# Optimization experiments

Hardware: AMD Instinct MI355X
Metric: run time of the kernel (lower is better)

The kernel has to match this reference:

```python
import jax, jax.numpy as jnp
import numpy as np

N = 100000      # nodes
E = 1600000     # edges
F_IN = 256      # num_features
H = 128         # hidden_dim
C = 16          # num_classes
LOG_SIGMA0 = float(np.log(0.1))  # prior_sigma = 0.1


def setup_inputs() -> dict:
    key = jax.random.key(0)
    ks = jax.random.split(key, 8)
    x = jax.random.normal(ks[0], (N, F_IN), jnp.float32)
    edge_index = jax.random.randint(ks[1], (2, E), 0, N, dtype=jnp.int64)
    # GCNConv linear weight + bias
    W = jax.random.normal(ks[2], (F_IN, H), jnp.float32) / np.float32(np.sqrt(F_IN))
    gcn_b = jnp.zeros((H,), jnp.float32)
    # BayesLinear params (mu + log_sigma) and fixed sampled noise eps
    w_mu = jax.random.normal(ks[3], (C, H), jnp.float32) / np.float32(np.sqrt(H))
    w_log_sigma = jnp.full((C, H), LOG_SIGMA0, jnp.float32)
    b_mu = jnp.zeros((C,), jnp.float32)
    b_log_sigma = jnp.full((C,), LOG_SIGMA0, jnp.float32)
    eps_w = jax.random.normal(ks[4], (C, H), jnp.float32)
    eps_b = jax.random.normal(ks[5], (C,), jnp.float32)
    return {"x": x, "edge_index": edge_index, "W": W, "gcn_b": gcn_b,
            "w_mu": w_mu, "w_log_sigma": w_log_sigma,
            "b_mu": b_mu, "b_log_sigma": b_log_sigma,
            "eps_w": eps_w, "eps_b": eps_b}


def reference(x, edge_index, W, gcn_b, w_mu, w_log_sigma, b_mu, b_log_sigma, eps_w, eps_b):
    n = x.shape[0]
    # --- GCNConv: add self-loops, symmetric deg^{-1/2} normalization ---
    loop = jnp.arange(n, dtype=edge_index.dtype)
    src = jnp.concatenate([edge_index[0], loop])  # message source j
    dst = jnp.concatenate([edge_index[1], loop])  # aggregation target i
    deg = jax.ops.segment_sum(jnp.ones_like(dst, dtype=x.dtype), dst, num_segments=n)
    deg_inv_sqrt = jnp.where(deg > 0, jax.lax.rsqrt(deg), 0.0)
    norm = deg_inv_sqrt[src] * deg_inv_sqrt[dst]            # [E+N]
    h = x @ W                                               # [N,H] transform first
    msg = h[src] * norm[:, None]                            # [E+N,H] gather
    agg = jax.ops.segment_sum(msg, dst, num_segments=n)     # [N,H] scatter-add
    agg = agg + gcn_b
    # --- ReLU; dropout is identity in eval mode ---
    a = jax.nn.relu(agg)
    # --- BayesLinear: w = mu + exp(log_sigma) * eps ---
    w = w_mu + jnp.exp(w_log_sigma) * eps_w                 # [C,H]
    b = b_mu + jnp.exp(b_log_sigma) * eps_b                 # [C]
    logits = a @ w.T + b                                    # [N,C]
    return jax.nn.log_softmax(logits, axis=1)
```

## Files before the change

### kernel.cpp

```cpp
#include <hip/hip_runtime.h>
#include <hip/hip_bf16.h>

#define N_NODES 100000
#define F_IN    256
#define H_DIM   128
#define C_CLS   16
#define NB_SCAN ((N_NODES + 255) / 256)
#define NSHARD  8
#define SHARD_W ((N_NODES + NSHARD - 1) / NSHARD)

typedef __attribute__((ext_vector_type(8))) short  short8;
typedef __attribute__((ext_vector_type(4))) float  float4v;
typedef __attribute__((ext_vector_type(4))) unsigned short ushort4v;

__device__ __forceinline__ float b2f(ushort u) {
    union { unsigned int i; float f; } v;
    v.i = ((unsigned int)u) << 16;
    return v.f;
}

__device__ __forceinline__ ushort f2b(float f) {
    unsigned int x = __float_as_uint(f);
    unsigned int r = (x + 0x7FFFu + ((x >> 16) & 1u)) >> 16;
    return (ushort)r;
}

__device__ __forceinline__ float ldsel(const void* p, int i, int f32f) {
    return f32f ? ((const float*)p)[i] : b2f(((const ushort*)p)[i]);
}

__global__ __launch_bounds__(64) void sniff(const ushort* __restrict__ x,
                                            const int* __restrict__ ei,
                                            int* __restrict__ flags) {
    int lane = threadIdx.x;
    int cnt_bf = 0;
#pragma unroll
    for (int j = 0; j < 4; ++j) {
        ushort u = x[lane * 4 + j];
        int e = (u >> 7) & 0xFF;
        if ((e >= 100 && e <= 140) || (u & 0x7FFF) == 0) cnt_bf++;
    }
    int zodd = (ei[2 * lane + 1] == 0) ? 1 : 0;
#pragma unroll
    for (int off = 32; off >= 1; off >>= 1) {
        cnt_bf += __shfl_xor(cnt_bf, off, 64);
        zodd   += __shfl_xor(zodd,   off, 64);
    }
    if (lane == 0) {
        flags[0] = (cnt_bf < 230) ? 1 : 0;
        flags[1] = (zodd  >= 32) ? 1 : 0;
    }
}

__global__ __launch_bounds__(256) void prep_params(const int* __restrict__ flags,
                                                   const void* __restrict__ W_any,
                                                   ushort* __restrict__ wtg,
                                                   const void* __restrict__ w_mu,
                                                   const void* __restrict__ w_ls,
                                                   const void* __restrict__ eps_w,
                                                   const void* __restrict__ b_mu,
                                                   const void* __restrict__ b_ls,
                                                   const void* __restrict__ eps_b,
                                                   const void* __restrict__ gcn_b,
                                                   ushort* __restrict__ whi,
                                                   ushort* __restrict__ wlo,
                                                   float* __restrict__ bias16,
                                                   float* __restrict__ gcnb_f) {
    const int f32f = flags[0];
    const int t = threadIdx.x;
    if (blockIdx.x < H_DIM) {
        const int n = blockIdx.x;
        float v = f32f ? ((const float*)W_any)[t * H_DIM + n]
                       : b2f(((const ushort*)W_any)[t * H_DIM + n]);
        wtg[n * F_IN + t] = f2b(v);
        return;
    }
#pragma unroll
    for (int i = t; i < C_CLS * H_DIM; i += 256) {
        float v = ldsel(w_mu, i, f32f) + __expf(ldsel(w_ls, i, f32f)) * ldsel(eps_w, i, f32f);
        ushort h = f2b(v);
        whi[i] = h;
        wlo[i] = f2b(v - b2f(h));
    }
    if (t < C_CLS)
        bias16[t] = ldsel(b_mu, t, f32f) + __expf(ldsel(b_ls, t, f32f)) * ldsel(eps_b, t, f32f);
    if (t < H_DIM)
        gcnb_f[t] = ldsel(gcn_b, t, f32f);
}

__global__ __launch_bounds__(256) void prep(const int* __restrict__ flags,
                                            const int* __restrict__ ei,
                                            int* __restrict__ cnt, int E) {
    int e = blockIdx.x * 256 + threadIdx.x;
    if (e >= E) return;
    int d = flags[1] ? ei[2L * E + 2L * e] : ei[(long)E + e];
    atomicAdd(&cnt[d], 1);
}

__global__ __launch_bounds__(256) void scan1(const int* __restrict__ cnt,
                                             int* __restrict__ offs,
                                             int* __restrict__ bsum) {
    __shared__ int sd[256];
    int t = threadIdx.x;
    int i = blockIdx.x * 256 + t;
    int v = (i < N_NODES) ? cnt[i] : 0;
    sd[t] = v;
    __syncthreads();
#pragma unroll
    for (int d = 1; d < 256; d <<= 1) {
        int add = (t >= d) ? sd[t - d] : 0;
        __syncthreads();
        sd[t] += add;
        __syncthreads();
    }
    if (i < N_NODES) offs[i] = sd[t] - v;
    if (t == 255) bsum[blockIdx.x] = sd[255];
}

__global__ __launch_bounds__(512) void scan2(const int* __restrict__ bsum,
                                             int* __restrict__ boff) {
    __shared__ int sd[512];
    int t = threadIdx.x;
    int v = (t < NB_SCAN) ? bsum[t] : 0;
    sd[t] = v;
    __syncthreads();
#pragma unroll
    for (int d = 1; d < 512; d <<= 1) {
        int add = (t >= d) ? sd[t - d] : 0;
        __syncthreads();
        sd[t] += add;
        __syncthreads();
    }
    if (t < NB_SCAN) boff[t] = sd[t] - v;
}

__global__ __launch_bounds__(256) void scan3(int* __restrict__ offs,
                                             const int* __restrict__ boff,
                                             const int* __restrict__ cnt,
                                             int* __restrict__ cursor,
                                             float* __restrict__ dis, int E) {
    int i = blockIdx.x * 256 + threadIdx.x;
    if (i == 0) offs[N_NODES] = E;
    if (i >= N_NODES) return;
    int off = offs[i] + boff[i >> 8];
    offs[i] = off;
    cursor[i] = off;
    dis[i] = rsqrtf((float)(cnt[i] + 1));
}

__global__ __launch_bounds__(256) void build_perm(const int* __restrict__ flags,
                                                  const int* __restrict__ ei,
                                                  int* __restrict__ cursor,
                                                  int* __restrict__ perm, int E) {
    const int shard = blockIdx.x & (NSHARD - 1);
    const int jb    = blockIdx.x >> 3;
    const int nb    = gridDim.x >> 3;
    const int lo = shard * SHARD_W;
    const int hi = lo + SHARD_W;
    const int i64 = flags[1];
    for (long e = (long)jb * 256 + threadIdx.x; e < E; e += (long)nb * 256) {
        int d = i64 ? ei[2L * E + 2L * e] : ei[(long)E + e];
        if (d >= lo && d < hi) {
            int s = i64 ? ei[2L * e] : ei[e];
            int slot = atomicAdd(&cursor[d], 1);
            perm[slot] = s;
        }
    }
}

__global__ __launch_bounds__(256) void gemm_xw(const int* __restrict__ flags,
                                               const void* __restrict__ x_any,
                                               const ushort* __restrict__ wtg,
                                               const float* __restrict__ dis,
                                               ushort* __restrict__ hout) {
    __shared__ __align__(16) ushort wt[128 * 128];
    const int f32f = flags[0];

    const int tid  = threadIdx.x;
    const int lane = tid & 63;
    const int quad = lane >> 4;
    const int lm   = lane & 15;
    const int wave = tid >> 6;

    const int rbase = blockIdx.x * 128 + wave * 32;
    int arow0 = rbase + lm;
    int arow1 = rbase + 16 + lm;
    if (arow0 >= N_NODES) arow0 = N_NODES - 1;
    if (arow1 >= N_NODES) arow1 = N_NODES - 1;
    const float*  xrf0 = (const float*) x_any + (size_t)arow0 * F_IN;
    const float*  xrf1 = (const float*) x_any + (size_t)arow1 * F_IN;
    const ushort* xrb0 = (const ushort*)x_any + (size_t)arow0 * F_IN;
    const ushort* xrb1 = (const ushort*)x_any + (size_t)arow1 * F_IN;

    float4v acc0[8], acc1[8];
#pragma unroll
    for (int c = 0; c < 8; ++c) {
        acc0[c] = (float4v){0.f, 0.f, 0.f, 0.f};
        acc1[c] = (float4v){0.f, 0.f, 0.f, 0.f};
    }

    for (int hh = 0; hh < 2; ++hh) {
        if (hh) __syncthreads();
#pragma unroll
        for (int it = 0; it < 8; ++it) {
            int flat = (it * 256 + tid) * 8;
            int col  = flat >> 7;
            int kloc = flat & 127;
            short8 v = *(const short8*)(wtg + col * F_IN + hh * 128 + kloc);
            int dst = ((col << 7) | kloc) ^ ((col & 7) << 3);
            *(short8*)(wt + dst) = v;
        }
        __syncthreads();
#pragma unroll
        for (int s = 0; s < 4; ++s) {
            int klocal = s * 32 + quad * 8;
            short8 afrag0, afrag1;
            if (f32f) {
                const float* p0 = xrf0 + hh * 128 + klocal;
                const float* p1 = xrf1 + hh * 128 + klocal;
                float4 u0 = *(const float4*)p0;
                float4 u1 = *(const float4*)(p0 + 4);
                float4 u2 = *(const float4*)p1;
                float4 u3 = *(const float4*)(p1 + 4);
                afrag0[0] = (short)f2b(u0.x); afrag0[1] = (short)f2b(u0.y);
                afrag0[2] = (short)f2b(u0.z); afrag0[3] = (short)f2b(u0.w);
                afrag0[4] = (short)f2b(u1.x); afrag0[5] = (short)f2b(u1.y);
                afrag0[6] = (short)f2b(u1.z); afrag0[7] = (short)f2b(u1.w);
                afrag1[0] = (short)f2b(u2.x); afrag1[1] = (short)f2b(u2.y);
                afrag1[2] = (short)f2b(u2.z); afrag1[3] = (short)f2b(u2.w);
                afrag1[4] = (short)f2b(u3.x); afrag1[5] = (short)f2b(u3.y);
                afrag1[6] = (short)f2b(u3.z); afrag1[7] = (short)f2b(u3.w);
            } else {
                afrag0 = *(const short8*)(xrb0 + hh * 128 + klocal);
                afrag1 = *(const short8*)(xrb1 + hh * 128 + klocal);
            }
#pragma unroll
            for (int c = 0; c < 8; ++c) {
                int colr = c * 16 + lm;
                int src = ((colr << 7) | klocal) ^ ((lm & 7) << 3);
                short8 bfrag = *(const short8*)(wt + src);
                acc0[c] = __builtin_amdgcn_mfma_f32_16x16x32_bf16(afrag0, bfrag, acc0[c], 0, 0, 0);
                acc1[c] = __builtin_amdgcn_mfma_f32_16x16x32_bf16(afrag1, bfrag, acc1[c], 0, 0, 0);
            }
        }
    }
    float dv0[4], dv1[4];
#pragma unroll
    for (int r = 0; r < 4; ++r) {
        int n0 = rbase + quad * 4 + r;
        int n1 = rbase + 16 + quad * 4 + r;
        dv0[r] = (n0 < N_NODES) ? dis[n0] : 0.f;
        dv1[r] = (n1 < N_NODES) ? dis[n1] : 0.f;
    }
#pragma unroll
    for (int c = 0; c < 8; ++c) {
        int col = c * 16 + lm;
#pragma unroll
        for (int r = 0; r < 4; ++r) {
            int n0 = rbase + quad * 4 + r;
            int n1 = rbase + 16 + quad * 4 + r;
            if (n0 < N_NODES) hout[(size_t)n0 * H_DIM + col] = f2b(acc0[c][r] * dv0[r]);
            if (n1 < N_NODES) hout[(size_t)n1 * H_DIM + col] = f2b(acc1[c][r] * dv1[r]);
        }
    }
}

__global__ __launch_bounds__(256) void gather_relu(const int* __restrict__ offs,
                                                   const int* __restrict__ perm,
                                                   const float* __restrict__ dis,
                                                   const ushort* __restrict__ hb,
                                                   const float* __restrict__ gcnb_f,
                                                   ushort* __restrict__ aout) {
    const int lane = threadIdx.x & 63;
    const int node = blockIdx.x * 4 + (threadIdx.x >> 6);
    if (node >= N_NODES) return;

    const int off0 = __builtin_amdgcn_readfirstlane(offs[node]);
    const int deg  = __builtin_amdgcn_readfirstlane(offs[node + 1]) - off0;
    const int* pp = perm + off0;

    float ax = 0.f, ay = 0.f;
    const int full = deg & ~15;
    for (int base = 0; base < full; base += 16) {
#pragma unroll
        for (int k = 0; k < 16; ++k) {
            int sk = pp[base + k];
            uint u = *((const uint*)(hb + (size_t)sk * H_DIM) + lane);
            ax += __uint_as_float(u << 16);
            ay += __uint_as_float(u & 0xFFFF0000u);
        }
    }
    {
        const int nb = deg - full;
#pragma unroll
        for (int k = 0; k < 16; ++k) {
            int   sk = 0;
            float wk = 0.f;
            if (k < nb) { sk = pp[full + k]; wk = 1.f; }
            uint u = *((const uint*)(hb + (size_t)sk * H_DIM) + lane);
            ax = fmaf(wk, __uint_as_float(u << 16),         ax);
            ay = fmaf(wk, __uint_as_float(u & 0xFFFF0000u), ay);
        }
    }

    const float dd = dis[node];
    uint us = *((const uint*)(hb + (size_t)node * H_DIM) + lane);
    float2 gb = *(const float2*)(gcnb_f + 2 * lane);
    ax = (ax + __uint_as_float(us << 16))         * dd + gb.x;
    ay = (ay + __uint_as_float(us & 0xFFFF0000u)) * dd + gb.y;
    ax = fmaxf(ax, 0.f);
    ay = fmaxf(ay, 0.f);
    uint pack = (uint)f2b(ax) | ((uint)f2b(ay) << 16);
    *((uint*)(aout + (size_t)node * H_DIM) + lane) = pack;
}

__global__ __launch_bounds__(256) void final_linear(const int* __restrict__ flags,
                                                    const ushort* __restrict__ a,
                                                    const ushort* __restrict__ whi,
                                                    const ushort* __restrict__ wlo,
                                                    const float* __restrict__ bias16,
                                                    void* __restrict__ out) {
    const int f32f = flags[0];
    const int lane = threadIdx.x & 63;
    const int wave = threadIdx.x >> 6;
    const int n0 = (blockIdx.x * 4 + wave) * 16;
    if (n0 >= N_NODES) return;
    const int lm = lane & 15, quad = lane >> 4;

    const ushort* arow = a   + (size_t)(n0 + lm) * H_DIM + quad * 8;
    const ushort* bh   = whi + lm * H_DIM + quad * 8;
    const ushort* bl   = wlo + lm * H_DIM + quad * 8;

    float4v acc = (float4v){0.f, 0.f, 0.f, 0.f};
#pragma unroll
    for (int s = 0; s < 4; ++s) {
        short8 af = *(const short8*)(arow + s * 32);
        short8 b0 = *(const short8*)(bh   + s * 32);
        short8 b1 = *(const short8*)(bl   + s * 32);
        acc = __builtin_amdgcn_mfma_f32_16x16x32_bf16(af, b0, acc, 0, 0, 0);
        acc = __builtin_amdgcn_mfma_f32_16x16x32_bf16(af, b1, acc, 0, 0, 0);
    }

    const float bias = bias16[lm];
    float p[4], m[4], ss[4];
#pragma unroll
    for (int r = 0; r < 4; ++r) { p[r] = acc[r] + bias; m[r] = p[r]; }
#pragma unroll
    for (int off = 1; off < 16; off <<= 1)
#pragma unroll
        for (int r = 0; r < 4; ++r) m[r] = fmaxf(m[r], __shfl_xor(m[r], off, 64));
#pragma unroll
    for (int r = 0; r < 4; ++r) ss[r] = __expf(p[r] - m[r]);
#pragma unroll
    for (int off = 1; off < 16; off <<= 1)
#pragma unroll
        for (int r = 0; r < 4; ++r) ss[r] += __shfl_xor(ss[r], off, 64);

    if (f32f) {
        float* op = (float*)out;
#pragma unroll
        for (int r = 0; r < 4; ++r)
            op[(size_t)(n0 + quad * 4 + r) * C_CLS + lm] = p[r] - m[r] - __logf(ss[r]);
    } else {
        ushort* op = (ushort*)out;
#pragma unroll
        for (int r = 0; r < 4; ++r)
            op[(size_t)(n0 + quad * 4 + r) * C_CLS + lm] = f2b(p[r] - m[r] - __logf(ss[r]));
    }
}

extern "C" void kernel_launch(void* const* d_in, const int* in_sizes, int n_in,
                              void* d_out, int out_size, void* d_ws, size_t ws_size,
                              hipStream_t stream) {
    const int E = in_sizes[1] / 2;

    char* wp = (char*)d_ws;
    auto alloc = [&](size_t bytes) -> char* {
        char* p = wp; wp += (bytes + 511) & ~(size_t)511; return p;
    };
    int*    flags  = (int*)   alloc(64);
    ushort* hb     = (ushort*)alloc((size_t)N_NODES * H_DIM * 2);
    ushort* aout   = (ushort*)alloc((size_t)N_NODES * H_DIM * 2);
    int*    cnt    = (int*)   alloc((size_t)N_NODES * 4);
    int*    offs   = (int*)   alloc((size_t)(N_NODES + 1) * 4);
    int*    cursor = (int*)   alloc((size_t)N_NODES * 4);
    int*    bsum   = (int*)   alloc((size_t)NB_SCAN * 4);
    int*    boff   = (int*)   alloc((size_t)NB_SCAN * 4);
    float*  dis    = (float*) alloc((size_t)N_NODES * 4);
    int*    perm   = (int*)   alloc((size_t)E * 4);
    ushort* wtg    = (ushort*)alloc((size_t)H_DIM * F_IN * 2);
    ushort* whi    = (ushort*)alloc((size_t)C_CLS * H_DIM * 2);
    ushort* wlo    = (ushort*)alloc((size_t)C_CLS * H_DIM * 2);
    float*  bias16 = (float*) alloc((size_t)C_CLS * 4);
    float*  gcnb_f = (float*) alloc((size_t)H_DIM * 4);

    sniff<<<1, 64, 0, stream>>>((const ushort*)d_in[0], (const int*)d_in[1], flags);
    prep_params<<<H_DIM + 1, 256, 0, stream>>>(flags, d_in[2], wtg,
                                  d_in[4], d_in[5], d_in[8],
                                  d_in[6], d_in[7], d_in[9], d_in[3],
                                  whi, wlo, bias16, gcnb_f);
    (void)hipMemsetAsync(cnt, 0, (size_t)N_NODES * 4, stream);
    prep<<<(E + 255) / 256, 256, 0, stream>>>(flags, (const int*)d_in[1], cnt, E);
    scan1<<<NB_SCAN, 256, 0, stream>>>(cnt, offs, bsum);
    scan2<<<1, 512, 0, stream>>>(bsum, boff);
    scan3<<<NB_SCAN, 256, 0, stream>>>(offs, boff, cnt, cursor, dis, E);
    build_perm<<<2048, 256, 0, stream>>>(flags, (const int*)d_in[1], cursor, perm, E);
    gemm_xw<<<(N_NODES + 127) / 128, 256, 0, stream>>>(flags, d_in[0], wtg, dis, hb);
    gather_relu<<<(N_NODES + 3) / 4, 256, 0, stream>>>(offs, perm, dis, hb, gcnb_f, aout);
    final_linear<<<(N_NODES / C_CLS + 3) / 4, 256, 0, stream>>>(flags, aout, whi, wlo, bias16, (void*)d_out);
}
```

Baseline: 414.5 us.

## Replace sharded perm build with two-pass shard binning then scatter

The old build_perm had each of eight shard groups re-read the whole edge list and keep only the edges whose destination fell in its node range. Now prep writes compacted (src,dst) pairs once. A new bin_pairs kernel buckets them by destination shard in LDS and flushes contiguous runs to per-shard segments. scatter_perm then reads only its own shard's segment to fill perm. This cuts the edge-list re-reads, at the cost of two extra E*8-byte buffers, an extra kernel launch and LDS-bound binning with frequent block syncs.

```diff
diff --git a/kernel.cpp b/kernel.cpp
--- a/kernel.cpp
+++ b/kernel.cpp
@@ -8,6 +8,8 @@
 #define NB_SCAN ((N_NODES + 255) / 256)
 #define NSHARD  8
 #define SHARD_W ((N_NODES + NSHARD - 1) / NSHARD)
+#define BINCAP  448
+#define FLUSH_THR 192
 
 typedef __attribute__((ext_vector_type(8))) short  short8;
 typedef __attribute__((ext_vector_type(4))) float  float4v;
@@ -90,10 +92,14 @@
 
 __global__ __launch_bounds__(256) void prep(const int* __restrict__ flags,
                                             const int* __restrict__ ei,
-                                            int* __restrict__ cnt, int E) {
+                                            int* __restrict__ cnt,
+                                            int2* __restrict__ pr, int E) {
     int e = blockIdx.x * 256 + threadIdx.x;
     if (e >= E) return;
-    int d = flags[1] ? ei[2L * E + 2L * e] : ei[(long)E + e];
+    int i64 = flags[1];
+    int s = i64 ? ei[2L * e]          : ei[e];
+    int d = i64 ? ei[2L * E + 2L * e] : ei[(long)E + e];
+    pr[e] = make_int2(s, d);
     atomicAdd(&cnt[d], 1);
 }
 
@@ -138,33 +144,75 @@
                                              const int* __restrict__ boff,
                                              const int* __restrict__ cnt,
                                              int* __restrict__ cursor,
-                                             float* __restrict__ dis, int E) {
+                                             float* __restrict__ dis,
+                                             int* __restrict__ tails, int E) {
     int i = blockIdx.x * 256 + threadIdx.x;
     if (i == 0) offs[N_NODES] = E;
     if (i >= N_NODES) return;
     int off = offs[i] + boff[i >> 8];
     offs[i] = off;
     cursor[i] = off;
+    if ((i % SHARD_W) == 0) tails[i / SHARD_W] = off;
     dis[i] = rsqrtf((float)(cnt[i] + 1));
 }
 
-__global__ __launch_bounds__(256) void build_perm(const int* __restrict__ flags,
-                                                  const int* __restrict__ ei,
-                                                  int* __restrict__ cursor,
-                                                  int* __restrict__ perm, int E) {
-    const int shard = blockIdx.x & (NSHARD - 1);
-    const int jb    = blockIdx.x >> 3;
-    const int nb    = gridDim.x >> 3;
-    const int lo = shard * SHARD_W;
-    const int hi = lo + SHARD_W;
-    const int i64 = flags[1];
-    for (long e = (long)jb * 256 + threadIdx.x; e < E; e += (long)nb * 256) {
-        int d = i64 ? ei[2L * E + 2L * e] : ei[(long)E + e];
-        if (d >= lo && d < hi) {
-            int s = i64 ? ei[2L * e] : ei[e];
-            int slot = atomicAdd(&cursor[d], 1);
-            perm[slot] = s;
-        }
+__global__ __launch_bounds__(256) void bin_pairs(const int2* __restrict__ pr,
+                                                 int* __restrict__ tails,
+                                                 int2* __restrict__ seg, int E) {
+    __shared__ int2 buf[NSHARD][BINCAP];
+    __shared__ int  bcnt[NSHARD], bbase[NSHARD], bflush[NSHARD];
+    const int t = threadIdx.x;
+    const long chunk = (E + gridDim.x - 1) / gridDim.x;
+    long lo  = (long)blockIdx.x * chunk;
+    long hiE = lo + chunk; if (hiE > E) hiE = E;
+    if (t < NSHARD) bcnt[t] = 0;
+    __syncthreads();
+    for (long base = lo; base < hiE; base += 256) {
+        long e = base + t;
+        if (e < hiE) {
+            int2 p = pr[e];
+            int sh = p.y / SHARD_W;
+            int pos = atomicAdd(&bcnt[sh], 1);
+            buf[sh][pos] = p;
+        }
+        __syncthreads();
+        const bool last = (base + 256 >= hiE);
+        if (t == 0) {
+#pragma unroll
+            for (int sh = 0; sh < NSHARD; ++sh) {
+                int n = bcnt[sh];
+                int f = (last || n >= FLUSH_THR) ? n : 0;
+                bflush[sh] = f;
+                if (f) bbase[sh] = atomicAdd(&tails[sh], f);
+            }
+        }
+        __syncthreads();
+#pragma unroll
+        for (int sh = 0; sh < NSHARD; ++sh) {
+            int f = bflush[sh];
+            if (f == 0) continue;
+            int b0 = bbase[sh];
+            for (int i = t; i < f; i += 256) seg[b0 + i] = buf[sh][i];
+        }
+        __syncthreads();
+        if (t < NSHARD && bflush[t]) bcnt[t] = 0;
+        __syncthreads();
+    }
+}
+
+__global__ __launch_bounds__(256) void scatter_perm(const int* __restrict__ offs,
+                                                    const int2* __restrict__ seg,
+                                                    int* __restrict__ cursor,
+                                                    int* __restrict__ perm) {
+    const int sh = blockIdx.x & (NSHARD - 1);
+    const int jb = blockIdx.x >> 3;
+    const int nb = gridDim.x >> 3;
+    const int lo = offs[sh * SHARD_W];
+    const int hi = offs[(sh + 1) * SHARD_W];
+    for (int e = lo + jb * 256 + threadIdx.x; e < hi; e += nb * 256) {
+        int2 p = seg[e];
+        int slot = atomicAdd(&cursor[p.y], 1);
+        perm[slot] = p.x;
     }
 }
 
@@ -388,6 +436,9 @@
     int*    boff   = (int*)   alloc((size_t)NB_SCAN * 4);
     float*  dis    = (float*) alloc((size_t)N_NODES * 4);
     int*    perm   = (int*)   alloc((size_t)E * 4);
+    int2*   pr     = (int2*)  alloc((size_t)E * 8);
+    int2*   seg    = (int2*)  alloc((size_t)E * 8);
+    int*    tails  = (int*)   alloc(64);
     ushort* wtg    = (ushort*)alloc((size_t)H_DIM * F_IN * 2);
     ushort* whi    = (ushort*)alloc((size_t)C_CLS * H_DIM * 2);
     ushort* wlo    = (ushort*)alloc((size_t)C_CLS * H_DIM * 2);
@@ -400,11 +451,12 @@
                                   d_in[6], d_in[7], d_in[9], d_in[3],
                                   whi, wlo, bias16, gcnb_f);
     (void)hipMemsetAsync(cnt, 0, (size_t)N_NODES * 4, stream);
-    prep<<<(E + 255) / 256, 256, 0, stream>>>(flags, (const int*)d_in[1], cnt, E);
+    prep<<<(E + 255) / 256, 256, 0, stream>>>(flags, (const int*)d_in[1], cnt, pr, E);
     scan1<<<NB_SCAN, 256, 0, stream>>>(cnt, offs, bsum);
     scan2<<<1, 512, 0, stream>>>(bsum, boff);
-    scan3<<<NB_SCAN, 256, 0, stream>>>(offs, boff, cnt, cursor, dis, E);
-    build_perm<<<2048, 256, 0, stream>>>(flags, (const int*)d_in[1], cursor, perm, E);
+    scan3<<<NB_SCAN, 256, 0, stream>>>(offs, boff, cnt, cursor, dis, tails, E);
+    bin_pairs<<<1024, 256, 0, stream>>>(pr, tails, seg, E);
+    scatter_perm<<<2048, 256, 0, stream>>>(offs, seg, cursor, perm);
     gemm_xw<<<(N_NODES + 127) / 128, 256, 0, stream>>>(flags, d_in[0], wtg, dis, hb);
     gather_relu<<<(N_NODES + 3) / 4, 256, 0, stream>>>(offs, perm, dis, hb, gcnb_f, aout);
     final_linear<<<(N_NODES / C_CLS + 3) / 4, 256, 0, stream>>>(flags, aout, whi, wlo, bias16, (void*)d_out);
```

New measurement: 565.7 us. 1.36x slower.
